# Performance work log

Measured on AMD Instinct MI355X. Metric: run time of the kernel, lower is better.

## Reference

```python
import jax, jax.numpy as jnp
import numpy as np
import math

B, C, N = 4, 128, 4096
GROUPS = 8
EPS = 1e-5


def setup_inputs() -> dict:
    key = jax.random.key(0)
    ks = jax.random.split(key, 7)
    x = jax.random.normal(ks[0], (B, C, N), dtype=jnp.float32)
    gn_w = jnp.ones((C,), dtype=jnp.float32)
    gn_b = jnp.zeros((C,), dtype=jnp.float32)
    # Conv1d with kernel_size=1 is a per-position linear map: weight [out, in]
    s_qkv = 1.0 / math.sqrt(C)
    w_qkv = jax.random.uniform(ks[1], (3 * C, C), jnp.float32, -s_qkv, s_qkv)
    b_qkv = jax.random.uniform(ks[2], (3 * C,), jnp.float32, -s_qkv, s_qkv)
    w_out = jax.random.uniform(ks[3], (C, C), jnp.float32, -s_qkv, s_qkv)
    b_out = jax.random.uniform(ks[4], (C,), jnp.float32, -s_qkv, s_qkv)
    return {"x": x, "gn_w": gn_w, "gn_b": gn_b, "w_qkv": w_qkv,
            "b_qkv": b_qkv, "w_out": w_out, "b_out": b_out}


def reference(x, gn_w, gn_b, w_qkv, b_qkv, w_out, b_out):
    b, c, n = x.shape
    # GroupNorm(8, c): normalize over (channels-in-group, n)
    xg = x.reshape(b, GROUPS, c // GROUPS, n)
    mean = jnp.mean(xg, axis=(2, 3), keepdims=True)
    var = jnp.var(xg, axis=(2, 3), keepdims=True)
    h = ((xg - mean) * jax.lax.rsqrt(var + EPS)).reshape(b, c, n)
    h = h * gn_w[None, :, None] + gn_b[None, :, None]
    # 1x1 conv QKV projection
    qkv = jnp.einsum('oc,bcn->bon', w_qkv, h) + b_qkv[None, :, None]
    q, k, v = jnp.split(qkv, 3, axis=1)  # each [b, c, n]
    scale = 1.0 / math.sqrt(c)
    attn = jax.nn.softmax(jnp.einsum('bci,bcj->bij', q, k) * scale, axis=-1)
    # h[b,c,i] = sum_j v[b,c,j] * attn[b,i,j]  (torch: bmm(v, attn^T))
    h2 = jnp.einsum('bcj,bij->bci', v, attn)
    out = jnp.einsum('oc,bcn->bon', w_out, h2) + b_out[None, :, None]
    return out + x
```

## Files before the change

kernel.cpp:

```cpp
#include <hip/hip_runtime.h>
#include <hip/hip_bf16.h>


#define CH 128
#define SEQ 4096
#define EPSV 1e-5f
#define QSCALE (0.08838834764831845f * 1.4426950408889634f)
#define SMAX 24.0f

typedef unsigned short u16;
typedef unsigned int u32;
typedef __attribute__((ext_vector_type(8))) short short8;
typedef __attribute__((ext_vector_type(4))) float floatx4;

__device__ __forceinline__ float bf2f(u16 h) {
    return __uint_as_float(((u32)h) << 16);
}
__device__ __forceinline__ u16 f2bf(float f) {
    u32 u = __float_as_uint(f);
    return (u16)((u + 0x7fffu + ((u >> 16) & 1u)) >> 16);
}
__device__ __forceinline__ u32 pkbf(float a, float b) {
    __hip_bfloat162 h = __float22bfloat162_rn(make_float2(a, b));
    return *(u32*)&h;
}
__device__ __forceinline__ floatx4 mfma16(short8 a, short8 b, floatx4 c) {
    return __builtin_amdgcn_mfma_f32_16x16x32_bf16(a, b, c, 0, 0, 0);
}

__global__ void gn_wconv(const float* __restrict__ x, float* __restrict__ part,
                         const float* __restrict__ w_qkv, const float* __restrict__ w_out,
                         u16* __restrict__ wq, u16* __restrict__ wo) {
    if (blockIdx.x >= 256) {
        int i = (blockIdx.x - 256) * 256 + threadIdx.x;
        if (i < 49152) wq[i] = f2bf(w_qkv[i]);
        else           wo[i - 49152] = f2bf(w_out[i - 49152]);
        return;
    }
    int bg = blockIdx.x >> 3, sub = blockIdx.x & 7;
    const float4* xp = (const float4*)(x + (size_t)bg * 65536 + sub * 8192);
    float s = 0.f, sq = 0.f;
    for (int r = 0; r < 8; ++r) {
        float4 v = xp[threadIdx.x + 256 * r];
        s  += v.x + v.y + v.z + v.w;
        sq += v.x*v.x + v.y*v.y + v.z*v.z + v.w*v.w;
    }
    for (int off = 32; off; off >>= 1) {
        s  += __shfl_down(s, off, 64);
        sq += __shfl_down(sq, off, 64);
    }
    __shared__ float ls[8];
    int wave = threadIdx.x >> 6, lane = threadIdx.x & 63;
    if (lane == 0) { ls[wave*2] = s; ls[wave*2+1] = sq; }
    __syncthreads();
    if (threadIdx.x == 0) {
        float ts = 0.f, tq = 0.f;
        for (int w = 0; w < 4; ++w) { ts += ls[w*2]; tq += ls[w*2+1]; }
        part[blockIdx.x * 2]     = ts;
        part[blockIdx.x * 2 + 1] = tq;
    }
}

__global__ __launch_bounds__(256, 2) void qkv_fused(
        const float* __restrict__ x, const float* __restrict__ gw,
        const float* __restrict__ gb, const float* __restrict__ part,
        const u16* __restrict__ wq, const float* __restrict__ b_qkv,
        u16* __restrict__ qT, u16* __restrict__ kT, u16* __restrict__ v) {
    __shared__ __align__(16) u16 hT[32 * 136];
    __shared__ __align__(16) u16 qbuf[32 * 132];
    __shared__ __align__(16) u16 kbuf[32 * 132];
    __shared__ __align__(16) u16 vbuf[128 * 36];
    __shared__ float cw[128], cb[128];
    int bx = blockIdx.x;
    int nc = bx & 127, b = bx >> 7;
    int n0 = nc * 32;
    int t = threadIdx.x, w = t >> 6, lane = t & 63;
    int quad = lane >> 4, l15 = lane & 15;

    if (t < 128) {
        int g = t >> 4;
        float s = 0.f, sq = 0.f;
        #pragma unroll
        for (int u = 0; u < 8; ++u) {
            s  += part[((b * 8 + g) * 8 + u) * 2];
            sq += part[((b * 8 + g) * 8 + u) * 2 + 1];
        }
        float mean = s / 65536.f;
        float rstd = rsqrtf(sq / 65536.f - mean * mean + EPSV);
        float wgt = gw[t] * rstd;
        cw[t] = wgt;
        cb[t] = gb[t] - mean * wgt;
    }

    short8 wf[6][4];
    float bqk[6];
    #pragma unroll
    for (int j = 0; j < 6; ++j) {
        int orow = (w * 6 + j) * 16 + l15;
        #pragma unroll
        for (int kt = 0; kt < 4; ++kt)
            wf[j][kt] = *(const short8*)(wq + orow * 128 + kt * 32 + quad * 8);
        bqk[j] = b_qkv[orow];
    }
    __syncthreads();

    #pragma unroll
    for (int r = 0; r < 4; ++r) {
        int u = r * 256 + t;
        int c = u >> 3, col = (u & 7) * 4;
        float wgt = cw[c], bs = cb[c];
        float4 xv = *(const float4*)(x + ((size_t)(b * 128 + c)) * SEQ + n0 + col);
        hT[(col + 0) * 136 + c] = f2bf(fmaf(xv.x, wgt, bs));
        hT[(col + 1) * 136 + c] = f2bf(fmaf(xv.y, wgt, bs));
        hT[(col + 2) * 136 + c] = f2bf(fmaf(xv.z, wgt, bs));
        hT[(col + 3) * 136 + c] = f2bf(fmaf(xv.w, wgt, bs));
    }
    __syncthreads();

    #pragma unroll
    for (int nt = 0; nt < 2; ++nt) {
        short8 hf[4];
        #pragma unroll
        for (int kt = 0; kt < 4; ++kt)
            hf[kt] = *(const short8*)(hT + (nt * 16 + l15) * 136 + kt * 32 + quad * 8);
        floatx4 acc[6];
        #pragma unroll
        for (int j = 0; j < 6; ++j) acc[j] = (floatx4)0.f;
        #pragma unroll
        for (int kt = 0; kt < 4; ++kt)
            #pragma unroll
            for (int j = 0; j < 6; ++j) {
                if (w * 6 + j < 16) acc[j] = mfma16(hf[kt], wf[j][kt], acc[j]);
                else                acc[j] = mfma16(wf[j][kt], hf[kt], acc[j]);
            }
        #pragma unroll
        for (int j = 0; j < 6; ++j) {
            int T = w * 6 + j;
            if (T < 8) {
                int o = T * 16 + l15;
                #pragma unroll
                for (int r = 0; r < 4; ++r)
                    qbuf[(nt * 16 + quad * 4 + r) * 132 + o] =
                        f2bf((acc[j][r] + bqk[j]) * QSCALE);
            } else if (T < 16) {
                int o = (T - 8) * 16 + l15;
                #pragma unroll
                for (int r = 0; r < 4; ++r)
                    kbuf[(nt * 16 + quad * 4 + r) * 132 + o] =
                        f2bf(acc[j][r] + bqk[j]);
            } else {
                #pragma unroll
                for (int r = 0; r < 4; ++r) {
                    int ov = (T - 16) * 16 + quad * 4 + r;
                    vbuf[ov * 36 + nt * 16 + l15] = f2bf(acc[j][r] + b_qkv[256 + ov]);
                }
            }
        }
    }
    __syncthreads();

    {
        u16* qg = qT + ((size_t)b * SEQ + n0) * CH;
        u16* kg = kT + ((size_t)b * SEQ + n0) * CH;
        #pragma unroll
        for (int rep = 0; rep < 2; ++rep) {
            int idx = rep * 256 + t;
            int n = idx >> 4, c8 = (idx & 15) * 8;
            *(uint4*)(qg + n * CH + c8) = *(const uint4*)(qbuf + n * 132 + c8);
            *(uint4*)(kg + n * CH + c8) = *(const uint4*)(kbuf + n * 132 + c8);
        }
        #pragma unroll
        for (int rep = 0; rep < 2; ++rep) {
            int idx = rep * 256 + t;
            int c = idx >> 2, n8 = (idx & 3) * 8;
            *(uint4*)(v + ((size_t)(b * CH + c)) * SEQ + n0 + n8) =
                *(const uint4*)(vbuf + c * 36 + n8);
        }
    }
}

__global__ __launch_bounds__(256, 2) void flash_attn(
        const u16* __restrict__ qT, const u16* __restrict__ kT,
        const u16* __restrict__ v, u16* __restrict__ partO,
        float* __restrict__ lbuf) {
    __shared__ __align__(16) char smem[54272];
    u16* kts = (u16*)smem;
    u16* vts = (u16*)(smem + 17408);
    u16* ps  = (u16*)(smem + 35840);
    u16* qts = (u16*)smem;

    int bx = blockIdx.x;
    int js = bx & 3, iblk = (bx >> 2) & 31, b = bx >> 7;
    int t = threadIdx.x, w = t >> 6, lane = t & 63;
    int quad = lane >> 4, l15 = lane & 15;
    int i0 = iblk * 128, j0 = js * 1024;

    {
        const u16* qb = qT + ((size_t)b * SEQ + i0) * CH;
        for (int r = 0; r < 8; ++r) {
            int u = r * 256 + t;
            int i = u >> 4, c16 = u & 15;
            *(uint4*)(qts + i * 136 + c16 * 8) =
                *(const uint4*)(qb + (size_t)i * CH + c16 * 8);
        }
    }
    __syncthreads();
    short8 qf[2][4];
    #pragma unroll
    for (int it = 0; it < 2; ++it)
        #pragma unroll
        for (int kt = 0; kt < 4; ++kt)
            qf[it][kt] = *(const short8*)(qts + (w * 32 + it * 16 + l15) * 136 + kt * 32 + quad * 8);

    float l_part[2] = {0.f, 0.f};
    floatx4 o[8][2];
    #pragma unroll
    for (int mt = 0; mt < 8; ++mt) { o[mt][0] = (floatx4)0.f; o[mt][1] = (floatx4)0.f; }

    const u16* kTb = kT + ((size_t)b * SEQ + j0) * CH;
    const u16* vb  = v  + (size_t)b * CH * SEQ + j0;

    for (int ch = 0; ch < 16; ++ch) {
        int jb = ch * 64;
        __syncthreads();
        for (int r = 0; r < 4; ++r) {
            int u = r * 256 + t;
            int j = u >> 4, c16 = u & 15;
            *(uint4*)(kts + j * 136 + c16 * 8) =
                *(const uint4*)(kTb + (size_t)(jb + j) * CH + c16 * 8);
        }
        for (int r = 0; r < 4; ++r) {
            int u = r * 256 + t;
            int c = u >> 3, col = u & 7;
            *(uint4*)(vts + c * 72 + col * 8) =
                *(const uint4*)(vb + (size_t)c * SEQ + jb + col * 8);
        }
        __syncthreads();

        floatx4 s[4][2];
        #pragma unroll
        for (int jt = 0; jt < 4; ++jt) { s[jt][0] = (floatx4)0.f; s[jt][1] = (floatx4)0.f; }
        #pragma unroll
        for (int jt = 0; jt < 4; ++jt)
            #pragma unroll
            for (int kt = 0; kt < 4; ++kt) {
                short8 kf = *(const short8*)(kts + (jt * 16 + l15) * 136 + kt * 32 + quad * 8);
                s[jt][0] = mfma16(kf, qf[0][kt], s[jt][0]);
                s[jt][1] = mfma16(kf, qf[1][kt], s[jt][1]);
            }

        #pragma unroll
        for (int it = 0; it < 2; ++it) {
            float lsum = 0.f;
            int rowoff = (w * 32 + it * 16 + l15) * 72 + quad * 4;
            #pragma unroll
            for (int jt = 0; jt < 4; ++jt) {
                float p0 = exp2f(s[jt][it][0] - SMAX);
                float p1 = exp2f(s[jt][it][1] - SMAX);
                float p2 = exp2f(s[jt][it][2] - SMAX);
                float p3 = exp2f(s[jt][it][3] - SMAX);
                lsum += (p0 + p1) + (p2 + p3);
                uint2 pk = make_uint2(pkbf(p0, p1), pkbf(p2, p3));
                *(uint2*)(ps + rowoff + jt * 16) = pk;
            }
            l_part[it] += lsum;
        }
        __builtin_amdgcn_wave_barrier();

        #pragma unroll
        for (int kt = 0; kt < 2; ++kt) {
            short8 pf0 = *(const short8*)(ps + (w * 32 + l15) * 72 + kt * 32 + quad * 8);
            short8 pf1 = *(const short8*)(ps + (w * 32 + 16 + l15) * 72 + kt * 32 + quad * 8);
            #pragma unroll
            for (int mt = 0; mt < 8; ++mt) {
                short8 vf = *(const short8*)(vts + (mt * 16 + l15) * 72 + kt * 32 + quad * 8);
                o[mt][0] = mfma16(vf, pf0, o[mt][0]);
                o[mt][1] = mfma16(vf, pf1, o[mt][1]);
            }
        }
    }

    int bi = b * 32 + iblk;
    u16* pb = partO + ((size_t)(js * 128 + bi)) * 16384;
    #pragma unroll
    for (int it = 0; it < 2; ++it) {
        int i = w * 32 + it * 16 + l15;
        #pragma unroll
        for (int mt = 0; mt < 8; ++mt) {
            uint2 pk = make_uint2(pkbf(o[mt][it][0], o[mt][it][1]),
                                  pkbf(o[mt][it][2], o[mt][it][3]));
            *(uint2*)(pb + i * 128 + mt * 16 + quad * 4) = pk;
        }
    }
    float* lb = lbuf + ((size_t)(js * 128 + bi)) * 128;
    #pragma unroll
    for (int it = 0; it < 2; ++it) {
        float l = l_part[it];
        l += __shfl_xor(l, 16, 64);
        l += __shfl_xor(l, 32, 64);
        if (lane < 16) lb[w * 32 + it * 16 + l15] = l;
    }
}

__global__ __launch_bounds__(256, 2) void merge_out(
        const u16* __restrict__ partO, const float* __restrict__ lbuf,
        const u16* __restrict__ wo, const float* __restrict__ b_out,
        const float* __restrict__ x, float* __restrict__ out) {
    __shared__ __align__(16) u16 h2T[32 * 136];
    __shared__ float fac[32];
    int bx = blockIdx.x;
    int qtr = bx & 3, iblk = (bx >> 2) & 31, b = bx >> 7;
    int bi = b * 32 + iblk;
    int i_base = qtr * 32;
    int t = threadIdx.x, w = t >> 6, lane = t & 63;
    int quad = lane >> 4, l15 = lane & 15;

    short8 wf[2][4];
    #pragma unroll
    for (int j = 0; j < 2; ++j)
        #pragma unroll
        for (int kt = 0; kt < 4; ++kt)
            wf[j][kt] = *(const short8*)(wo + ((w * 2 + j) * 16 + l15) * 128 + kt * 32 + quad * 8);

    if (t < 32) {
        int i = i_base + t;
        float lv = 0.f;
        #pragma unroll
        for (int s = 0; s < 4; ++s)
            lv += lbuf[((size_t)(s * 128 + bi)) * 128 + i];
        fac[t] = 1.f / lv;
    }
    __syncthreads();

    {
        int il = t >> 3, oct = t & 7;
        int i = i_base + il;
        float accv[16];
        #pragma unroll
        for (int e = 0; e < 16; ++e) accv[e] = 0.f;
        for (int s = 0; s < 4; ++s) {
            const u16* pb = partO + ((size_t)(s * 128 + bi)) * 16384
                            + i * 128 + oct * 16;
            u16 a[16];
            *(uint4*)(a)     = *(const uint4*)(pb);
            *(uint4*)(a + 8) = *(const uint4*)(pb + 8);
            #pragma unroll
            for (int e = 0; e < 16; ++e) accv[e] += bf2f(a[e]);
        }
        float fs = fac[il];
        #pragma unroll
        for (int e = 0; e < 16; ++e) accv[e] *= fs;
        uint4 lo = make_uint4(pkbf(accv[0],  accv[1]),  pkbf(accv[2],  accv[3]),
                              pkbf(accv[4],  accv[5]),  pkbf(accv[6],  accv[7]));
        uint4 hi = make_uint4(pkbf(accv[8],  accv[9]),  pkbf(accv[10], accv[11]),
                              pkbf(accv[12], accv[13]), pkbf(accv[14], accv[15]));
        *(uint4*)(h2T + il * 136 + oct * 16)     = lo;
        *(uint4*)(h2T + il * 136 + oct * 16 + 8) = hi;
    }
    __syncthreads();

    floatx4 acc[2][2];
    #pragma unroll
    for (int j = 0; j < 2; ++j) { acc[j][0] = (floatx4)0.f; acc[j][1] = (floatx4)0.f; }
    #pragma unroll
    for (int nt = 0; nt < 2; ++nt)
        #pragma unroll
        for (int kt = 0; kt < 4; ++kt) {
            short8 hf = *(const short8*)(h2T + (nt * 16 + l15) * 136 + kt * 32 + quad * 8);
            acc[0][nt] = mfma16(wf[0][kt], hf, acc[0][nt]);
            acc[1][nt] = mfma16(wf[1][kt], hf, acc[1][nt]);
        }

    int n_base = iblk * 128 + i_base;
    #pragma unroll
    for (int j = 0; j < 2; ++j)
        #pragma unroll
        for (int r = 0; r < 4; ++r) {
            int o = w * 32 + j * 16 + quad * 4 + r;
            float bo = b_out[o];
            #pragma unroll
            for (int nt = 0; nt < 2; ++nt) {
                int n = n_base + nt * 16 + l15;
                size_t idx = ((size_t)(b * 128 + o)) * SEQ + n;
                out[idx] = acc[j][nt][r] + bo + x[idx];
            }
        }
}

extern "C" void kernel_launch(void* const* d_in, const int* in_sizes, int n_in,
                              void* d_out, int out_size, void* d_ws, size_t ws_size,
                              hipStream_t stream) {
    const float* x     = (const float*)d_in[0];
    const float* gn_w  = (const float*)d_in[1];
    const float* gn_b  = (const float*)d_in[2];
    const float* w_qkv = (const float*)d_in[3];
    const float* b_qkv = (const float*)d_in[4];
    const float* w_out = (const float*)d_in[5];
    const float* b_out = (const float*)d_in[6];
    float* out = (float*)d_out;

    char* ws = (char*)d_ws;
    float* part = (float*)ws;
    u16*  wq  = (u16*)(ws + 4096);
    u16*  wo  = (u16*)(ws + 102400);
    u16*  qT  = (u16*)(ws + 135168);
    u16*  kT  = (u16*)(ws + 4329472);
    u16*  v   = (u16*)(ws + 8523776);
    u16*  pO  = (u16*)(ws + 12718080);
    float* lb = (float*)(ws + 29495296);

    gn_wconv<<<512, 256, 0, stream>>>(x, part, w_qkv, w_out, wq, wo);
    qkv_fused<<<512, 256, 0, stream>>>(x, gn_w, gn_b, part, wq, b_qkv, qT, kT, v);
    flash_attn<<<512, 256, 0, stream>>>(qT, kT, v, pO, lb);
    merge_out<<<512, 256, 0, stream>>>(pO, lb, wo, b_out, x, out);
}
```

Measured before the change: 83.47 us.

## Use 32x32 MFMA with in-register P via permlane swap and 8-way KV split

```diff
diff --git a/kernel.cpp b/kernel.cpp
--- a/kernel.cpp
+++ b/kernel.cpp
@@ -12,6 +12,7 @@
 typedef unsigned int u32;
 typedef __attribute__((ext_vector_type(8))) short short8;
 typedef __attribute__((ext_vector_type(4))) float floatx4;
+typedef __attribute__((ext_vector_type(16))) float floatx16;
 
 __device__ __forceinline__ float bf2f(u16 h) {
     return __uint_as_float(((u32)h) << 16);
@@ -26,6 +27,17 @@
 }
 __device__ __forceinline__ floatx4 mfma16(short8 a, short8 b, floatx4 c) {
     return __builtin_amdgcn_mfma_f32_16x16x32_bf16(a, b, c, 0, 0, 0);
+}
+__device__ __forceinline__ floatx16 mfma32(short8 a, short8 b, floatx16 c) {
+    return __builtin_amdgcn_mfma_f32_32x32x16_bf16(a, b, c, 0, 0, 0);
+}
+__device__ __forceinline__ void pl32(u32& a, u32& b) {
+    asm volatile("v_permlane32_swap_b32 %0, %1" : "+v"(a), "+v"(b));
+}
+__device__ __forceinline__ short8 mk8(u32 a, u32 b, u32 c, u32 d) {
+    union { u32 u[4]; short8 s; } t;
+    t.u[0] = a; t.u[1] = b; t.u[2] = c; t.u[3] = d;
+    return t.s;
 }
 
 __global__ void gn_wconv(const float* __restrict__ x, float* __restrict__ part,
@@ -179,21 +191,24 @@
     }
 }
 
-__global__ __launch_bounds__(256, 2) void flash_attn(
+__global__ __launch_bounds__(256, 3) void flash_attn(
         const u16* __restrict__ qT, const u16* __restrict__ kT,
         const u16* __restrict__ v, u16* __restrict__ partO,
-        float* __restrict__ lbuf) {
-    __shared__ __align__(16) char smem[54272];
+        float* __restrict__ lbuf, int jsbits) {
+    __shared__ __align__(16) char smem[35840];
     u16* kts = (u16*)smem;
     u16* vts = (u16*)(smem + 17408);
-    u16* ps  = (u16*)(smem + 35840);
     u16* qts = (u16*)smem;
 
     int bx = blockIdx.x;
-    int js = bx & 3, iblk = (bx >> 2) & 31, b = bx >> 7;
+    int js = bx & ((1 << jsbits) - 1);
+    int iblk = (bx >> jsbits) & 31;
+    int b = bx >> (jsbits + 5);
     int t = threadIdx.x, w = t >> 6, lane = t & 63;
-    int quad = lane >> 4, l15 = lane & 15;
-    int i0 = iblk * 128, j0 = js * 1024;
+    int il = lane & 31, h = lane >> 5;
+    int i0 = iblk * 128;
+    int j0 = js << (12 - jsbits);
+    int nchunk = 64 >> jsbits;
 
     {
         const u16* qb = qT + ((size_t)b * SEQ + i0) * CH;
@@ -205,22 +220,20 @@
         }
     }
     __syncthreads();
-    short8 qf[2][4];
-    #pragma unroll
-    for (int it = 0; it < 2; ++it)
-        #pragma unroll
-        for (int kt = 0; kt < 4; ++kt)
-            qf[it][kt] = *(const short8*)(qts + (w * 32 + it * 16 + l15) * 136 + kt * 32 + quad * 8);
-
-    float l_part[2] = {0.f, 0.f};
-    floatx4 o[8][2];
-    #pragma unroll
-    for (int mt = 0; mt < 8; ++mt) { o[mt][0] = (floatx4)0.f; o[mt][1] = (floatx4)0.f; }
+    short8 qf[8];
+    #pragma unroll
+    for (int kc = 0; kc < 8; ++kc)
+        qf[kc] = *(const short8*)(qts + (w * 32 + il) * 136 + kc * 16 + h * 8);
+
+    float l_part = 0.f;
+    floatx16 o[4];
+    #pragma unroll
+    for (int ct = 0; ct < 4; ++ct) o[ct] = (floatx16)0.f;
 
     const u16* kTb = kT + ((size_t)b * SEQ + j0) * CH;
     const u16* vb  = v  + (size_t)b * CH * SEQ + j0;
 
-    for (int ch = 0; ch < 16; ++ch) {
+    for (int ch = 0; ch < nchunk; ++ch) {
         int jb = ch * 64;
         __syncthreads();
         for (int r = 0; r < 4; ++r) {
@@ -237,75 +250,64 @@
         }
         __syncthreads();
 
-        floatx4 s[4][2];
-        #pragma unroll
-        for (int jt = 0; jt < 4; ++jt) { s[jt][0] = (floatx4)0.f; s[jt][1] = (floatx4)0.f; }
-        #pragma unroll
-        for (int jt = 0; jt < 4; ++jt)
-            #pragma unroll
-            for (int kt = 0; kt < 4; ++kt) {
-                short8 kf = *(const short8*)(kts + (jt * 16 + l15) * 136 + kt * 32 + quad * 8);
-                s[jt][0] = mfma16(kf, qf[0][kt], s[jt][0]);
-                s[jt][1] = mfma16(kf, qf[1][kt], s[jt][1]);
+        #pragma unroll
+        for (int jt = 0; jt < 2; ++jt) {
+            floatx16 s = (floatx16)(-SMAX);
+            __builtin_amdgcn_s_setprio(1);
+            #pragma unroll
+            for (int kc = 0; kc < 8; ++kc) {
+                short8 kf = *(const short8*)(kts + (jt * 32 + il) * 136 + kc * 16 + h * 8);
+                s = mfma32(kf, qf[kc], s);
             }
-
-        #pragma unroll
-        for (int it = 0; it < 2; ++it) {
-            float lsum = 0.f;
-            int rowoff = (w * 32 + it * 16 + l15) * 72 + quad * 4;
-            #pragma unroll
-            for (int jt = 0; jt < 4; ++jt) {
-                float p0 = exp2f(s[jt][it][0] - SMAX);
-                float p1 = exp2f(s[jt][it][1] - SMAX);
-                float p2 = exp2f(s[jt][it][2] - SMAX);
-                float p3 = exp2f(s[jt][it][3] - SMAX);
-                lsum += (p0 + p1) + (p2 + p3);
-                uint2 pk = make_uint2(pkbf(p0, p1), pkbf(p2, p3));
-                *(uint2*)(ps + rowoff + jt * 16) = pk;
+            __builtin_amdgcn_s_setprio(0);
+
+            float p[16];
+            #pragma unroll
+            for (int r = 0; r < 16; ++r) p[r] = __builtin_amdgcn_exp2f(s[r]);
+            l_part += ((((p[0]+p[1])+(p[2]+p[3])) + ((p[4]+p[5])+(p[6]+p[7])))
+                    +  (((p[8]+p[9])+(p[10]+p[11])) + ((p[12]+p[13])+(p[14]+p[15]))));
+
+            u32 a0 = pkbf(p[0],  p[1]),  a1 = pkbf(p[2],  p[3]);
+            u32 a2 = pkbf(p[4],  p[5]),  a3 = pkbf(p[6],  p[7]);
+            u32 b0 = pkbf(p[8],  p[9]),  b1 = pkbf(p[10], p[11]);
+            u32 b2 = pkbf(p[12], p[13]), b3 = pkbf(p[14], p[15]);
+            pl32(a0, a2); pl32(a1, a3);
+            pl32(b0, b2); pl32(b1, b3);
+            short8 pf0 = mk8(a0, a1, a2, a3);
+            short8 pf1 = mk8(b0, b1, b2, b3);
+
+            __builtin_amdgcn_s_setprio(1);
+            #pragma unroll
+            for (int ct = 0; ct < 4; ++ct) {
+                short8 vf0 = *(const short8*)(vts + (ct * 32 + il) * 72 + jt * 32 + h * 8);
+                short8 vf1 = *(const short8*)(vts + (ct * 32 + il) * 72 + jt * 32 + 16 + h * 8);
+                o[ct] = mfma32(vf0, pf0, o[ct]);
+                o[ct] = mfma32(vf1, pf1, o[ct]);
             }
-            l_part[it] += lsum;
-        }
-        __builtin_amdgcn_wave_barrier();
-
-        #pragma unroll
-        for (int kt = 0; kt < 2; ++kt) {
-            short8 pf0 = *(const short8*)(ps + (w * 32 + l15) * 72 + kt * 32 + quad * 8);
-            short8 pf1 = *(const short8*)(ps + (w * 32 + 16 + l15) * 72 + kt * 32 + quad * 8);
-            #pragma unroll
-            for (int mt = 0; mt < 8; ++mt) {
-                short8 vf = *(const short8*)(vts + (mt * 16 + l15) * 72 + kt * 32 + quad * 8);
-                o[mt][0] = mfma16(vf, pf0, o[mt][0]);
-                o[mt][1] = mfma16(vf, pf1, o[mt][1]);
-            }
+            __builtin_amdgcn_s_setprio(0);
         }
     }
 
     int bi = b * 32 + iblk;
-    u16* pb = partO + ((size_t)(js * 128 + bi)) * 16384;
-    #pragma unroll
-    for (int it = 0; it < 2; ++it) {
-        int i = w * 32 + it * 16 + l15;
-        #pragma unroll
-        for (int mt = 0; mt < 8; ++mt) {
-            uint2 pk = make_uint2(pkbf(o[mt][it][0], o[mt][it][1]),
-                                  pkbf(o[mt][it][2], o[mt][it][3]));
-            *(uint2*)(pb + i * 128 + mt * 16 + quad * 4) = pk;
-        }
-    }
-    float* lb = lbuf + ((size_t)(js * 128 + bi)) * 128;
-    #pragma unroll
-    for (int it = 0; it < 2; ++it) {
-        float l = l_part[it];
-        l += __shfl_xor(l, 16, 64);
-        l += __shfl_xor(l, 32, 64);
-        if (lane < 16) lb[w * 32 + it * 16 + l15] = l;
-    }
+    int i_loc = w * 32 + il;
+    u16* pb = partO + ((size_t)(js * 128 + bi)) * 16384 + i_loc * 128;
+    #pragma unroll
+    for (int ct = 0; ct < 4; ++ct)
+        #pragma unroll
+        for (int g = 0; g < 4; ++g) {
+            uint2 pk2 = make_uint2(pkbf(o[ct][4*g+0], o[ct][4*g+1]),
+                                   pkbf(o[ct][4*g+2], o[ct][4*g+3]));
+            *(uint2*)(pb + ct * 32 + 8 * g + 4 * h) = pk2;
+        }
+    l_part += __shfl_xor(l_part, 32, 64);
+    if (lane < 32)
+        lbuf[((size_t)(js * 128 + bi)) * 128 + i_loc] = l_part;
 }
 
 __global__ __launch_bounds__(256, 2) void merge_out(
         const u16* __restrict__ partO, const float* __restrict__ lbuf,
         const u16* __restrict__ wo, const float* __restrict__ b_out,
-        const float* __restrict__ x, float* __restrict__ out) {
+        const float* __restrict__ x, float* __restrict__ out, int nsplit) {
     __shared__ __align__(16) u16 h2T[32 * 136];
     __shared__ float fac[32];
     int bx = blockIdx.x;
@@ -325,8 +327,7 @@
     if (t < 32) {
         int i = i_base + t;
         float lv = 0.f;
-        #pragma unroll
-        for (int s = 0; s < 4; ++s)
+        for (int s = 0; s < nsplit; ++s)
             lv += lbuf[((size_t)(s * 128 + bi)) * 128 + i];
         fac[t] = 1.f / lv;
     }
@@ -338,7 +339,7 @@
         float accv[16];
         #pragma unroll
         for (int e = 0; e < 16; ++e) accv[e] = 0.f;
-        for (int s = 0; s < 4; ++s) {
+        for (int s = 0; s < nsplit; ++s) {
             const u16* pb = partO + ((size_t)(s * 128 + bi)) * 16384
                             + i * 128 + oct * 16;
             u16 a[16];
@@ -406,11 +407,16 @@
     u16*  qT  = (u16*)(ws + 135168);
     u16*  kT  = (u16*)(ws + 4329472);
     u16*  v   = (u16*)(ws + 8523776);
+
+    int nsplit = 8, jsbits = 3;
+    size_t need8 = 12718080ull + 33554432ull + 524288ull;
+    if (ws_size < need8) { nsplit = 4; jsbits = 2; }
+    size_t poBytes = (size_t)nsplit * 128 * 16384 * 2;
     u16*  pO  = (u16*)(ws + 12718080);
-    float* lb = (float*)(ws + 29495296);
+    float* lb = (float*)(ws + 12718080 + poBytes);
 
     gn_wconv<<<512, 256, 0, stream>>>(x, part, w_qkv, w_out, wq, wo);
     qkv_fused<<<512, 256, 0, stream>>>(x, gn_w, gn_b, part, wq, b_qkv, qT, kT, v);
-    flash_attn<<<512, 256, 0, stream>>>(qT, kT, v, pO, lb);
-    merge_out<<<512, 256, 0, stream>>>(pO, lb, wo, b_out, x, out);
-}
+    flash_attn<<<128 * nsplit, 256, 0, stream>>>(qT, kT, v, pO, lb, jsbits);
+    merge_out<<<512, 256, 0, stream>>>(pO, lb, wo, b_out, x, out, nsplit);
+}
```

Result: slower. 150.1 us (+79.9%).
